# Kernel tuning notes

Measured on AMD Instinct MI355X. Metric: run time of the kernel, lower is better.

Reference implementation:

```python
import jax, jax.numpy as jnp
import numpy as np

N, E = 100000, 400000
IN_CH, OUT_CH, HEADS, TIME_DIM, MSG_DIM = 100, 100, 2, 100, 100
EDGE_DIM = MSG_DIM + TIME_DIM  # 200
MEAN_DT, STD_DT = 0.0, 1.0


def setup_inputs() -> dict:
    key = jax.random.key(0)
    ks = jax.random.split(key, 16)
    HC = HEADS * OUT_CH
    s_in = 1.0 / np.sqrt(IN_CH)
    s_e = 1.0 / np.sqrt(EDGE_DIM)
    return {
        "x": jax.random.normal(ks[0], (N, IN_CH), jnp.float32),
        "last_update": jax.random.uniform(ks[1], (N,), jnp.float32) * 1000.0,
        "edge_index": jax.random.randint(ks[2], (2, E), 0, N, jnp.int32),
        "t": jax.random.uniform(ks[3], (E,), jnp.float32) * 1000.0,
        "msg": jax.random.normal(ks[4], (E, MSG_DIM), jnp.float32),
        "w_time": jax.random.normal(ks[5], (TIME_DIM,), jnp.float32),
        "b_time": jax.random.normal(ks[6], (TIME_DIM,), jnp.float32) * 0.1,
        "Wq": jax.random.normal(ks[7], (IN_CH, HC), jnp.float32) * s_in,
        "bq": jnp.zeros((HC,), jnp.float32),
        "Wk": jax.random.normal(ks[8], (IN_CH, HC), jnp.float32) * s_in,
        "bk": jnp.zeros((HC,), jnp.float32),
        "Wv": jax.random.normal(ks[9], (IN_CH, HC), jnp.float32) * s_in,
        "bv": jnp.zeros((HC,), jnp.float32),
        "We": jax.random.normal(ks[10], (EDGE_DIM, HC), jnp.float32) * s_e,  # lin_edge (no bias in PyG)
        "Ws": jax.random.normal(ks[11], (IN_CH, HC), jnp.float32) * s_in,   # lin_skip (root weight)
        "bs": jnp.zeros((HC,), jnp.float32),
    }


def reference(x, last_update, edge_index, t, msg, w_time, b_time,
              Wq, bq, Wk, bk, Wv, bv, We, Ws, bs):
    n = x.shape[0]
    src, dst = edge_index[0], edge_index[1]
    # relative time encoding: cos(Linear(1 -> TIME_DIM))
    rel_t = jnp.abs(last_update[src] - t)
    rel_t = (rel_t - MEAN_DT) / STD_DT
    t_enc = jnp.cos(rel_t[:, None] * w_time[None, :] + b_time)  # [E, TIME_DIM]
    edge_attr = jnp.concatenate([t_enc, msg], axis=-1)          # [E, EDGE_DIM]

    # TransformerConv (heads=2, concat=True, root_weight=True; dropout off in eval)
    q = (x @ Wq + bq).reshape(n, HEADS, OUT_CH)                 # [N,H,C]
    k = ((x @ Wk + bk)[src]).reshape(-1, HEADS, OUT_CH)         # [E,H,C]
    v = ((x @ Wv + bv)[src]).reshape(-1, HEADS, OUT_CH)
    e = (edge_attr @ We).reshape(-1, HEADS, OUT_CH)
    k = k + e
    v = v + e

    alpha = jnp.einsum('ehc,ehc->eh', q[dst], k) / np.sqrt(OUT_CH)  # [E,H]
    # segment softmax over incoming edges of each dst node
    amax = jax.ops.segment_max(alpha, dst, num_segments=n)          # [N,H]
    ex = jnp.exp(alpha - amax[dst])
    denom = jax.ops.segment_sum(ex, dst, num_segments=n)            # [N,H]
    attn = ex / (denom[dst] + 1e-16)                                # [E,H]

    out = jax.ops.segment_sum(v * attn[..., None], dst, num_segments=n)  # [N,H,C]
    out = out.reshape(n, HEADS * OUT_CH) + (x @ Ws + bs)
    return out
```

## Files before the change

### kernel.cpp

```cpp
#include <hip/hip_runtime.h>
#include <math.h>

#define N_NODES 100000
#define N_EDGES 400000
#define IN_CH   100
#define OUT_CH  100
#define HEADS   2
#define HC      200
#define TIME_DIM 100
#define MSG_DIM  100
#define EDGE_DIM 200
#define KP_NODE 128
#define KP_EDGE 224
#define NP_EDGE 208
#define PAD_HC  256
#define EW      264
#define NSLAB_ELEMS (13 * 16 * KP_NODE)
#define W4T_ELEMS   (4 * NSLAB_ELEMS)
#define M_CHUNK 128
#define NCHUNK  782

typedef __attribute__((ext_vector_type(8))) short bf16x8_t;
typedef __attribute__((ext_vector_type(4))) float f32x4_t;

struct __align__(8) us4 { unsigned short x, y, z, w; };

static __device__ __forceinline__ float b2f(unsigned short u){
  union { float f; unsigned int i; } v; v.i = ((unsigned int)u) << 16; return v.f;
}
static __device__ __forceinline__ unsigned short f2b(float f){
  union { float f; unsigned int i; } v; v.f = f;
  unsigned int x = v.i;
  return (unsigned short)((x + 0x7fffu + ((x >> 16) & 1u)) >> 16);
}

static __device__ __forceinline__ float fast_cos(float x){
  float r = x * 0.15915494309189535f;
  r = __builtin_amdgcn_fractf(r);
  return __builtin_amdgcn_cosf(r);
}

#define LDS_FENCE() do { \
  asm volatile("s_waitcnt lgkmcnt(0)" ::: "memory"); \
  __builtin_amdgcn_sched_barrier(0); \
} while (0)

__global__ __launch_bounds__(256) void pack_weights(
    const float* __restrict__ Wq, const float* __restrict__ bq,
    const float* __restrict__ Wk, const float* __restrict__ bk,
    const float* __restrict__ Wv, const float* __restrict__ bv,
    const float* __restrict__ We, const float* __restrict__ Ws, const float* __restrict__ bs,
    unsigned short* __restrict__ W4T, unsigned short* __restrict__ WeT,
    float* __restrict__ bias4)
{
  int idx = blockIdx.x * 256 + threadIdx.x;
  if (idx < W4T_ELEMS) {
    int row = idx >> 7;
    int k   = idx & 127;
    int t = row >> 4, j = row & 15;
    int slab = t / 13, i = t % 13;
    int col = i * 16 + j;
    float v = 0.f;
    if (k < IN_CH && col < HC) {
      const float* W = (slab == 0) ? Wq : (slab == 1) ? Wk : (slab == 2) ? Wv : Ws;
      v = W[k * HC + col];
    }
    W4T[idx] = f2b(v);
    return;
  }
  int j = idx - W4T_ELEMS;
  if (j < NP_EDGE * KP_EDGE) {
    int n = j / KP_EDGE, k = j % KP_EDGE;
    float v = 0.f;
    if (n < HC && k < EDGE_DIM) v = We[k * HC + n];
    WeT[j] = f2b(v);
    return;
  }
  j -= NP_EDGE * KP_EDGE;
  if (j < 4 * 208) {
    int slab = j / 208, col = j % 208;
    const float* B = (slab == 0) ? bq : (slab == 1) ? bk : (slab == 2) ? bv : bs;
    bias4[j] = (col < HC) ? B[col] : 0.f;
  }
}

__global__ __launch_bounds__(256) void node_gemm(
    const float* __restrict__ x, const unsigned short* __restrict__ W4T,
    const float* __restrict__ bias4,
    unsigned short* __restrict__ q_b, unsigned short* __restrict__ k_b,
    unsigned short* __restrict__ v_b, float* __restrict__ out)
{
  __shared__ __align__(16) unsigned char smem[34816];
  unsigned short* xt = (unsigned short*)smem;

  const int tid   = threadIdx.x;
  const int slab  = blockIdx.x & 3;
  const int chunk = blockIdx.x >> 2;
  const int n0    = chunk * M_CHUNK;
  const int nrows = (N_NODES - n0 < M_CHUNK) ? (N_NODES - n0) : M_CHUNK;

  const int lane = tid & 63, wave = tid >> 6;
  const int m16 = lane & 15, quad = lane >> 4;
  const int rb = wave * 32;

  for (int idx = lane; idx < 800; idx += 64) {
    int r = idx / 25, j = (idx % 25) * 4;
    int gr = rb + r;
    unsigned short* dst = xt + gr * 136 + j;
    if (gr < nrows) {
      float4 xv = *reinterpret_cast<const float4*>(x + (size_t)(n0 + gr) * IN_CH + j);
      dst[0] = f2b(xv.x); dst[1] = f2b(xv.y); dst[2] = f2b(xv.z); dst[3] = f2b(xv.w);
    } else {
      us4 z = {0, 0, 0, 0};
      *reinterpret_cast<us4*>(dst) = z;
    }
  }
  for (int idx = lane; idx < 224; idx += 64) {
    int r = idx / 7, j = idx % 7;
    us4 z = {0, 0, 0, 0};
    *reinterpret_cast<us4*>(&xt[(rb + r) * 136 + 100 + j * 4]) = z;
  }
  LDS_FENCE();

  float bias_v[13];
  #pragma unroll
  for (int i = 0; i < 13; i++) bias_v[i] = bias4[slab * 208 + i * 16 + m16];

  f32x4_t acc[2][13];
  #pragma unroll
  for (int s = 0; s < 2; s++)
    #pragma unroll
    for (int i = 0; i < 13; i++) acc[s][i] = (f32x4_t){0.f, 0.f, 0.f, 0.f};

  const unsigned short* Wp = W4T + (size_t)slab * NSLAB_ELEMS;
  for (int kc = 0; kc < 4; kc++) {
    bf16x8_t a0 = *reinterpret_cast<const bf16x8_t*>(&xt[(rb + m16) * 136 + kc * 32 + quad * 8]);
    bf16x8_t a1 = *reinterpret_cast<const bf16x8_t*>(&xt[(rb + 16 + m16) * 136 + kc * 32 + quad * 8]);
    #pragma unroll
    for (int i = 0; i < 13; i++) {
      bf16x8_t b = *reinterpret_cast<const bf16x8_t*>(
          &Wp[(size_t)(i * 16 + m16) * KP_NODE + kc * 32 + quad * 8]);
      acc[0][i] = __builtin_amdgcn_mfma_f32_16x16x32_bf16(a0, b, acc[0][i], 0, 0, 0);
      acc[1][i] = __builtin_amdgcn_mfma_f32_16x16x32_bf16(a1, b, acc[1][i], 0, 0, 0);
    }
  }

  unsigned short* stg  = xt + rb * 136;
  float*          stgf = (float*)stg;

  if (slab < 2) {
    unsigned short* gb = (slab == 0) ? q_b : k_b;
    for (int s = 0; s < 2; s++) {
      LDS_FENCE();
      for (int idx = lane; idx < 224; idx += 64) {
        int r = idx / 14, j = idx % 14;
        int col = (j < 7) ? (100 + j * 4) : (228 + (j - 7) * 4);
        us4 z = {0, 0, 0, 0};
        *reinterpret_cast<us4*>(&stg[r * 256 + col]) = z;
      }
      #pragma unroll
      for (int i = 0; i < 13; i++) {
        int c = i * 16 + m16;
        if (c < 200) {
          int pc = (c < 100) ? c : c + 28;
          #pragma unroll
          for (int r = 0; r < 4; r++)
            stg[(quad * 4 + r) * 256 + pc] = f2b(acc[s][i][r] + bias_v[i]);
        }
      }
      LDS_FENCE();
      const int rbase = rb + s * 16;
      uint4* g = (uint4*)(gb + (size_t)(n0 + rbase) * PAD_HC);
      const uint4* sv = (const uint4*)stg;
      for (int idx = lane; idx < 512; idx += 64)
        if (rbase + (idx >> 5) < nrows) g[idx] = sv[idx];
    }
  } else if (slab == 2) {
    for (int s = 0; s < 2; s++) {
      LDS_FENCE();
      #pragma unroll
      for (int i = 0; i < 13; i++) {
        int c = i * 16 + m16;
        if (c < 200) {
          #pragma unroll
          for (int r = 0; r < 4; r++)
            stg[(quad * 4 + r) * 200 + c] = f2b(acc[s][i][r] + bias_v[i]);
        }
      }
      LDS_FENCE();
      const int rbase = rb + s * 16;
      uint4* g = (uint4*)(v_b + (size_t)(n0 + rbase) * HC);
      const uint4* sv = (const uint4*)stg;
      for (int idx = lane; idx < 400; idx += 64)
        if (rbase + idx / 25 < nrows) g[idx] = sv[idx];
    }
  } else {
    for (int r8 = 0; r8 < 4; r8++) {
      const int s = r8 >> 1;
      LDS_FENCE();
      if ((quad >> 1) == (r8 & 1)) {
        int lr = (quad & 1) * 4;
        #pragma unroll
        for (int i = 0; i < 13; i++) {
          int c = i * 16 + m16;
          if (c < 200) {
            #pragma unroll
            for (int r = 0; r < 4; r++)
              stgf[(lr + r) * 200 + c] = acc[s][i][r] + bias_v[i];
          }
        }
      }
      LDS_FENCE();
      const int rbase = rb + r8 * 8;
      uint4* g = (uint4*)(out + (size_t)(n0 + rbase) * HC);
      const uint4* sv = (const uint4*)stgf;
      for (int idx = lane; idx < 400; idx += 64)
        if (rbase + idx / 50 < nrows) g[idx] = sv[idx];
    }
  }
}

__global__ __launch_bounds__(256, 4) void edge_gemm(
    const int* __restrict__ edge_index, const float* __restrict__ t,
    const float* __restrict__ last_update, const float* __restrict__ msg,
    const float* __restrict__ w_time, const float* __restrict__ b_time,
    const unsigned short* __restrict__ WeT,
    const unsigned short* __restrict__ q_b, const unsigned short* __restrict__ k_b,
    const unsigned short* __restrict__ v_b,
    unsigned short* __restrict__ v_e, float* __restrict__ exbuf)
{
  __shared__ __align__(16) unsigned short e_lds[64 * EW];
  __shared__ int   src_s[64], dst_s[64];
  __shared__ float rel_s[64], wt_s[TIME_DIM], bt_s[TIME_DIM];

  const int tid = threadIdx.x;
  const int e0 = blockIdx.x * 64;

  if (tid < TIME_DIM) { wt_s[tid] = w_time[tid]; bt_s[tid] = b_time[tid]; }
  else if (tid >= 128 && tid < 192) {
    int el = tid - 128; int e = e0 + el;
    int s = edge_index[e], d = edge_index[N_EDGES + e];
    src_s[el] = s; dst_s[el] = d;
    rel_s[el] = fabsf(last_update[s] - t[e]);
  }
  __syncthreads();

  const int lane = tid & 63, wave = tid >> 6;
  const int m16 = lane & 15, quad = lane >> 4;
  const int r0 = wave * 16;
  unsigned short* my = e_lds + r0 * EW;

  const int my_src = src_s[r0 + m16];
  const int my_dst = dst_s[r0 + m16];
  bf16x8_t kpre[2][4];
  #pragma unroll
  for (int h = 0; h < 2; h++)
    #pragma unroll
    for (int kc = 0; kc < 4; kc++)
      kpre[h][kc] = *reinterpret_cast<const bf16x8_t*>(
          &k_b[(size_t)my_src * PAD_HC + h * 128 + kc * 32 + quad * 8]);

  for (int it = 0; it < 14; it++) {
    int idx = it * 64 + lane;
    int row = idx / 56, c4 = (idx % 56) * 4;
    us4 o;
    if (c4 < TIME_DIM) {
      float rel = rel_s[r0 + row];
      o.x = f2b(fast_cos(rel * wt_s[c4 + 0] + bt_s[c4 + 0]));
      o.y = f2b(fast_cos(rel * wt_s[c4 + 1] + bt_s[c4 + 1]));
      o.z = f2b(fast_cos(rel * wt_s[c4 + 2] + bt_s[c4 + 2]));
      o.w = f2b(fast_cos(rel * wt_s[c4 + 3] + bt_s[c4 + 3]));
    } else if (c4 < EDGE_DIM) {
      float4 m = *reinterpret_cast<const float4*>(
          msg + (size_t)(e0 + r0 + row) * MSG_DIM + (c4 - TIME_DIM));
      o.x = f2b(m.x); o.y = f2b(m.y); o.z = f2b(m.z); o.w = f2b(m.w);
    } else {
      o.x = o.y = o.z = o.w = 0;
    }
    *reinterpret_cast<us4*>(&my[row * EW + c4]) = o;
  }
  __syncthreads();

  f32x4_t acc[4][4];
  #pragma unroll
  for (int i = 0; i < 4; i++)
    #pragma unroll
    for (int m = 0; m < 4; m++) acc[i][m] = (f32x4_t){0.f, 0.f, 0.f, 0.f};

  #pragma unroll
  for (int i = 0; i < 4; i++) {
    const int nt = wave + 4 * i;
    if (nt < 13) {
      for (int kc = 0; kc < 7; kc++) {
        bf16x8_t b = *reinterpret_cast<const bf16x8_t*>(
            &WeT[(nt * 16 + m16) * KP_EDGE + kc * 32 + quad * 8]);
        #pragma unroll
        for (int m = 0; m < 4; m++) {
          bf16x8_t a = *reinterpret_cast<const bf16x8_t*>(
              &e_lds[(m * 16 + m16) * EW + kc * 32 + quad * 8]);
          acc[i][m] = __builtin_amdgcn_mfma_f32_16x16x32_bf16(a, b, acc[i][m], 0, 0, 0);
        }
      }
    }
  }
  __syncthreads();

  #pragma unroll
  for (int i = 0; i < 4; i++) {
    const int nt = wave + 4 * i;
    if (nt < 13) {
      int c = nt * 16 + m16;
      if (c < 200) {
        int pc = (c < 100) ? c : c + 28;
        #pragma unroll
        for (int m = 0; m < 4; m++)
          #pragma unroll
          for (int r = 0; r < 4; r++)
            e_lds[(m * 16 + quad * 4 + r) * EW + pc] = f2b(acc[i][m][r]);
      }
    }
  }
  for (int idx = lane; idx < 224; idx += 64) {
    int row = idx / 14, j = idx % 14;
    int col = (j < 7) ? (100 + j * 4) : (228 + (j - 7) * 4);
    us4 z = {0, 0, 0, 0};
    *reinterpret_cast<us4*>(&my[row * EW + col]) = z;
  }
  __syncthreads();

  f32x4_t dacc[2];
  dacc[0] = (f32x4_t){0.f, 0.f, 0.f, 0.f};
  dacc[1] = (f32x4_t){0.f, 0.f, 0.f, 0.f};
  #pragma unroll
  for (int h = 0; h < 2; h++) {
    #pragma unroll
    for (int kc = 0; kc < 4; kc++) {
      int ko = h * 128 + kc * 32 + quad * 8;
      bf16x8_t a  = *reinterpret_cast<const bf16x8_t*>(&q_b[(size_t)my_dst * PAD_HC + ko]);
      bf16x8_t eb = *reinterpret_cast<const bf16x8_t*>(&my[m16 * EW + ko]);
      dacc[h] = __builtin_amdgcn_mfma_f32_16x16x32_bf16(a, kpre[h][kc], dacc[h], 0, 0, 0);
      dacc[h] = __builtin_amdgcn_mfma_f32_16x16x32_bf16(a, eb, dacc[h], 0, 0, 0);
    }
  }
  if (quad == (m16 >> 2)) {
    int r = m16 & 3;
    int e = e0 + r0 + m16;
    exbuf[(size_t)e * 2 + 0] = expf(dacc[0][r] * 0.1f);
    exbuf[(size_t)e * 2 + 1] = expf(dacc[1][r] * 0.1f);
  }

  for (int idx = lane; idx < 800; idx += 64) {
    int row = idx / 50, c = (idx % 50) * 4;
    int pc = (c < 100) ? c : c + 28;
    us4 ev = *reinterpret_cast<const us4*>(&my[row * EW + pc]);
    us4 vv = *reinterpret_cast<const us4*>(&v_b[(size_t)src_s[r0 + row] * HC + c]);
    us4 o;
    o.x = f2b(b2f(ev.x) + b2f(vv.x));
    o.y = f2b(b2f(ev.y) + b2f(vv.y));
    o.z = f2b(b2f(ev.z) + b2f(vv.z));
    o.w = f2b(b2f(ev.w) + b2f(vv.w));
    *reinterpret_cast<us4*>(&v_e[(size_t)(e0 + r0 + row) * HC + c]) = o;
  }
}

__global__ __launch_bounds__(256) void hist_kernel(const int* __restrict__ edge_index,
                                                   int* __restrict__ deg)
{
  int e = blockIdx.x * 256 + threadIdx.x;
  if (e < N_EDGES) atomicAdd(&deg[edge_index[N_EDGES + e]], 1);
}

__global__ __launch_bounds__(256) void scan1(const int* __restrict__ deg,
                                             int* __restrict__ cursor, int* __restrict__ bsum)
{
  __shared__ int s[256];
  const int tid = threadIdx.x;
  const int base = blockIdx.x * 1024 + tid * 4;
  int v[4]; int sum = 0;
  #pragma unroll
  for (int j = 0; j < 4; j++) {
    int i = base + j;
    v[j] = (i < N_NODES) ? deg[i] : 0;
    sum += v[j];
  }
  s[tid] = sum; __syncthreads();
  for (int d = 1; d < 256; d <<= 1) {
    int y = (tid >= d) ? s[tid - d] : 0;
    __syncthreads();
    s[tid] += y;
    __syncthreads();
  }
  int excl = s[tid] - sum;
  if (tid == 255) bsum[blockIdx.x] = s[255];
  int run = excl;
  #pragma unroll
  for (int j = 0; j < 4; j++) {
    int i = base + j;
    if (i < N_NODES) cursor[i] = run;
    run += v[j];
  }
}

__global__ void scan2(int* __restrict__ bsum, int nb)
{
  if (threadIdx.x == 0) {
    int acc = 0;
    for (int i = 0; i < nb; i++) { int t = bsum[i]; bsum[i] = acc; acc += t; }
  }
}

__global__ __launch_bounds__(256) void scan3(int* __restrict__ cursor,
                                             const int* __restrict__ bsum)
{
  int i = blockIdx.x * 256 + threadIdx.x;
  if (i < N_NODES) cursor[i] += bsum[i >> 10];
}

__global__ __launch_bounds__(256) void fill_csr(const int* __restrict__ edge_index,
                                                int* __restrict__ cursor, int* __restrict__ csr)
{
  int e = blockIdx.x * 256 + threadIdx.x;
  if (e < N_EDGES) {
    int p = atomicAdd(&cursor[edge_index[N_EDGES + e]], 1);
    csr[p] = e;
  }
}

__global__ __launch_bounds__(256) void gather_out(
    const int* __restrict__ cursor ,
    const int* __restrict__ deg, const int* __restrict__ csr,
    const unsigned short* __restrict__ v_e, const float* __restrict__ exbuf,
    float* __restrict__ out)
{
  const int wave = threadIdx.x >> 6, lane = threadIdx.x & 63;
  const int n = blockIdx.x * 4 + wave;
  const int dg = deg[n];
  const int off = cursor[n] - dg;

  float d0 = 1e-16f, d1 = 1e-16f;
  for (int j = 0; j < dg; j++) {
    int e = csr[off + j];
    d0 += exbuf[(size_t)e * 2 + 0];
    d1 += exbuf[(size_t)e * 2 + 1];
  }
  const float i0 = 1.f / d0, i1 = 1.f / d1;

  const int c0 = lane, c1 = lane + 64, c2 = lane + 128, c3 = lane + 192;
  float a0 = 0.f, a1 = 0.f, a2 = 0.f, a3 = 0.f;
  for (int j = 0; j < dg; j++) {
    int e = csr[off + j];
    float w0 = exbuf[(size_t)e * 2 + 0] * i0;
    float w1 = exbuf[(size_t)e * 2 + 1] * i1;
    const unsigned short* vr = v_e + (size_t)e * HC;
    a0 += ((c0 < 100) ? w0 : w1) * b2f(vr[c0]);
    a1 += ((c1 < 100) ? w0 : w1) * b2f(vr[c1]);
    a2 += w1 * b2f(vr[c2]);
    if (c3 < HC) a3 += w1 * b2f(vr[c3]);
  }
  float* o = out + (size_t)n * HC;
  o[c0] += a0; o[c1] += a1; o[c2] += a2;
  if (c3 < HC) o[c3] += a3;
}

extern "C" void kernel_launch(void* const* d_in, const int* in_sizes, int n_in,
                              void* d_out, int out_size, void* d_ws, size_t ws_size,
                              hipStream_t stream)
{
  const float* x           = (const float*)d_in[0];
  const float* last_update = (const float*)d_in[1];
  const int*   edge_index  = (const int*)  d_in[2];
  const float* t           = (const float*)d_in[3];
  const float* msg         = (const float*)d_in[4];
  const float* w_time      = (const float*)d_in[5];
  const float* b_time      = (const float*)d_in[6];
  const float* Wq = (const float*)d_in[7];  const float* bq = (const float*)d_in[8];
  const float* Wk = (const float*)d_in[9];  const float* bk = (const float*)d_in[10];
  const float* Wv = (const float*)d_in[11]; const float* bv = (const float*)d_in[12];
  const float* We = (const float*)d_in[13];
  const float* Ws = (const float*)d_in[14]; const float* bs = (const float*)d_in[15];
  float* out = (float*)d_out;

  char* ws = (char*)d_ws;
  size_t off = 0;
  auto alloc = [&](size_t bytes) -> void* {
    void* p = ws + off;
    off = (off + bytes + 255) & ~(size_t)255;
    return p;
  };
  unsigned short* W4T   = (unsigned short*)alloc((size_t)W4T_ELEMS * 2);
  unsigned short* WeT   = (unsigned short*)alloc((size_t)NP_EDGE * KP_EDGE * 2);
  float*          bias4 = (float*)         alloc((size_t)4 * 208 * 4);
  unsigned short* q_b   = (unsigned short*)alloc((size_t)N_NODES * PAD_HC * 2);
  unsigned short* k_b   = (unsigned short*)alloc((size_t)N_NODES * PAD_HC * 2);
  unsigned short* v_b   = (unsigned short*)alloc((size_t)N_NODES * HC * 2);
  unsigned short* v_e   = (unsigned short*)alloc((size_t)N_EDGES * HC * 2);
  float*          exbuf = (float*)         alloc((size_t)N_EDGES * 2 * 4);
  int*            deg   = (int*)           alloc((size_t)N_NODES * 4);
  int*            cursor= (int*)           alloc((size_t)N_NODES * 4);
  int*            bsum  = (int*)           alloc((size_t)128 * 4);
  int*            csr   = (int*)           alloc((size_t)N_EDGES * 4);

  hipMemsetAsync(deg, 0, (size_t)N_NODES * 4, stream);

  {
    int total = W4T_ELEMS + NP_EDGE * KP_EDGE + 4 * 208;
    pack_weights<<<(total + 255) / 256, 256, 0, stream>>>(
        Wq, bq, Wk, bk, Wv, bv, We, Ws, bs, W4T, WeT, bias4);
  }
  hist_kernel<<<(N_EDGES + 255) / 256, 256, 0, stream>>>(edge_index, deg);
  const int nb = (N_NODES + 1023) / 1024;
  scan1<<<nb, 256, 0, stream>>>(deg, cursor, bsum);
  scan2<<<1, 64, 0, stream>>>(bsum, nb);
  scan3<<<(N_NODES + 255) / 256, 256, 0, stream>>>(cursor, bsum);

  node_gemm<<<NCHUNK * 4, 256, 0, stream>>>(x, W4T, bias4, q_b, k_b, v_b, out);
  edge_gemm<<<N_EDGES / 64, 256, 0, stream>>>(
      edge_index, t, last_update, msg, w_time, b_time, WeT, q_b, k_b, v_b,
      v_e, exbuf);
  fill_csr<<<(N_EDGES + 255) / 256, 256, 0, stream>>>(edge_index, cursor, csr);
  gather_out<<<N_NODES / 4, 256, 0, stream>>>(cursor, deg, csr, v_e, exbuf, out);
}
```

Before: 917.3 us.

## Scatter edge outputs into CSR order and fuse softmax denominator into gather

The CSR position of each edge is now computed before edge_gemm, and edge_gemm writes v_e and exbuf rows directly at that position. gather_out then reads contiguous rows instead of going through the csr indirection. It also does the denominator sum and the weighted accumulation in a single pass, normalizing at the end. The cost is that edge_gemm's stores are scattered instead of sequential, while the gather's reads become contiguous and one pass over exbuf is saved.

```diff
diff --git a/kernel.cpp b/kernel.cpp
--- a/kernel.cpp
+++ b/kernel.cpp
@@ -226,11 +226,11 @@
     const float* __restrict__ w_time, const float* __restrict__ b_time,
     const unsigned short* __restrict__ WeT,
     const unsigned short* __restrict__ q_b, const unsigned short* __restrict__ k_b,
-    const unsigned short* __restrict__ v_b,
+    const unsigned short* __restrict__ v_b, const int* __restrict__ pos,
     unsigned short* __restrict__ v_e, float* __restrict__ exbuf)
 {
   __shared__ __align__(16) unsigned short e_lds[64 * EW];
-  __shared__ int   src_s[64], dst_s[64];
+  __shared__ int   src_s[64], dst_s[64], pos_s[64];
   __shared__ float rel_s[64], wt_s[TIME_DIM], bt_s[TIME_DIM];
 
   const int tid = threadIdx.x;
@@ -241,6 +241,7 @@
     int el = tid - 128; int e = e0 + el;
     int s = edge_index[e], d = edge_index[N_EDGES + e];
     src_s[el] = s; dst_s[el] = d;
+    pos_s[el] = pos[e];
     rel_s[el] = fabsf(last_update[s] - t[e]);
   }
   __syncthreads();
@@ -344,9 +345,9 @@
   }
   if (quad == (m16 >> 2)) {
     int r = m16 & 3;
-    int e = e0 + r0 + m16;
-    exbuf[(size_t)e * 2 + 0] = expf(dacc[0][r] * 0.1f);
-    exbuf[(size_t)e * 2 + 1] = expf(dacc[1][r] * 0.1f);
+    size_t p = (size_t)pos_s[r0 + m16];
+    exbuf[p * 2 + 0] = expf(dacc[0][r] * 0.1f);
+    exbuf[p * 2 + 1] = expf(dacc[1][r] * 0.1f);
   }
 
   for (int idx = lane; idx < 800; idx += 64) {
@@ -359,7 +360,7 @@
     o.y = f2b(b2f(ev.y) + b2f(vv.y));
     o.z = f2b(b2f(ev.z) + b2f(vv.z));
     o.w = f2b(b2f(ev.w) + b2f(vv.w));
-    *reinterpret_cast<us4*>(&v_e[(size_t)(e0 + r0 + row) * HC + c]) = o;
+    *reinterpret_cast<us4*>(&v_e[(size_t)pos_s[r0 + row] * HC + c]) = o;
   }
 }
 
@@ -417,18 +418,18 @@
 }
 
 __global__ __launch_bounds__(256) void fill_csr(const int* __restrict__ edge_index,
-                                                int* __restrict__ cursor, int* __restrict__ csr)
+                                                int* __restrict__ cursor, int* __restrict__ pos)
 {
   int e = blockIdx.x * 256 + threadIdx.x;
   if (e < N_EDGES) {
     int p = atomicAdd(&cursor[edge_index[N_EDGES + e]], 1);
-    csr[p] = e;
+    pos[e] = p;
   }
 }
 
 __global__ __launch_bounds__(256) void gather_out(
     const int* __restrict__ cursor ,
-    const int* __restrict__ deg, const int* __restrict__ csr,
+    const int* __restrict__ deg,
     const unsigned short* __restrict__ v_e, const float* __restrict__ exbuf,
     float* __restrict__ out)
 {
@@ -438,28 +439,25 @@
   const int off = cursor[n] - dg;
 
   float d0 = 1e-16f, d1 = 1e-16f;
-  for (int j = 0; j < dg; j++) {
-    int e = csr[off + j];
-    d0 += exbuf[(size_t)e * 2 + 0];
-    d1 += exbuf[(size_t)e * 2 + 1];
-  }
-  const float i0 = 1.f / d0, i1 = 1.f / d1;
-
   const int c0 = lane, c1 = lane + 64, c2 = lane + 128, c3 = lane + 192;
   float a0 = 0.f, a1 = 0.f, a2 = 0.f, a3 = 0.f;
   for (int j = 0; j < dg; j++) {
-    int e = csr[off + j];
-    float w0 = exbuf[(size_t)e * 2 + 0] * i0;
-    float w1 = exbuf[(size_t)e * 2 + 1] * i1;
-    const unsigned short* vr = v_e + (size_t)e * HC;
-    a0 += ((c0 < 100) ? w0 : w1) * b2f(vr[c0]);
-    a1 += ((c1 < 100) ? w0 : w1) * b2f(vr[c1]);
-    a2 += w1 * b2f(vr[c2]);
-    if (c3 < HC) a3 += w1 * b2f(vr[c3]);
-  }
+    size_t p = (size_t)(off + j);
+    float ex0 = exbuf[p * 2 + 0];
+    float ex1 = exbuf[p * 2 + 1];
+    d0 += ex0; d1 += ex1;
+    const unsigned short* vr = v_e + p * HC;
+    a0 += ((c0 < 100) ? ex0 : ex1) * b2f(vr[c0]);
+    a1 += ((c1 < 100) ? ex0 : ex1) * b2f(vr[c1]);
+    a2 += ex1 * b2f(vr[c2]);
+    if (c3 < HC) a3 += ex1 * b2f(vr[c3]);
+  }
+  const float i0 = 1.f / d0, i1 = 1.f / d1;
   float* o = out + (size_t)n * HC;
-  o[c0] += a0; o[c1] += a1; o[c2] += a2;
-  if (c3 < HC) o[c3] += a3;
+  o[c0] += a0 * ((c0 < 100) ? i0 : i1);
+  o[c1] += a1 * ((c1 < 100) ? i0 : i1);
+  o[c2] += a2 * i1;
+  if (c3 < HC) o[c3] += a3 * i1;
 }
 
 extern "C" void kernel_launch(void* const* d_in, const int* in_sizes, int n_in,
@@ -498,7 +496,7 @@
   int*            deg   = (int*)           alloc((size_t)N_NODES * 4);
   int*            cursor= (int*)           alloc((size_t)N_NODES * 4);
   int*            bsum  = (int*)           alloc((size_t)128 * 4);
-  int*            csr   = (int*)           alloc((size_t)N_EDGES * 4);
+  int*            pos   = (int*)           alloc((size_t)N_EDGES * 4);
 
   hipMemsetAsync(deg, 0, (size_t)N_NODES * 4, stream);
 
@@ -512,11 +510,11 @@
   scan1<<<nb, 256, 0, stream>>>(deg, cursor, bsum);
   scan2<<<1, 64, 0, stream>>>(bsum, nb);
   scan3<<<(N_NODES + 255) / 256, 256, 0, stream>>>(cursor, bsum);
+  fill_csr<<<(N_EDGES + 255) / 256, 256, 0, stream>>>(edge_index, cursor, pos);
 
   node_gemm<<<NCHUNK * 4, 256, 0, stream>>>(x, W4T, bias4, q_b, k_b, v_b, out);
   edge_gemm<<<N_EDGES / 64, 256, 0, stream>>>(
-      edge_index, t, last_update, msg, w_time, b_time, WeT, q_b, k_b, v_b,
+      edge_index, t, last_update, msg, w_time, b_time, WeT, q_b, k_b, v_b, pos,
       v_e, exbuf);
-  fill_csr<<<(N_EDGES + 255) / 256, 256, 0, stream>>>(edge_index, cursor, csr);
-  gather_out<<<N_NODES / 4, 256, 0, stream>>>(cursor, deg, csr, v_e, exbuf, out);
-}
+  gather_out<<<N_NODES / 4, 256, 0, stream>>>(cursor, deg, v_e, exbuf, out);
+}
```

Result: faster. 848.4 us (-7.5%).
